# Optimization experiments

Measured on AMD Instinct MI355X. Metric: run time of the kernel, lower is better.

Reference implementation:

```python
import jax, jax.numpy as jnp
import numpy as np

GRID_MIN, GRID_MAX, NUM_GRIDS = -2.0, 2.0, 15
DENOM = (GRID_MAX - GRID_MIN) / (NUM_GRIDS - 1)
LN_EPS = 1e-3  # tf.keras LayerNormalization default epsilon


def setup_inputs() -> dict:
    key = jax.random.key(0)
    k_x, k_sw, k_bw = jax.random.split(key, 3)
    N, D = 32768, 512
    G = NUM_GRIDS
    x = jax.random.normal(k_x, (N, D), dtype=jnp.float32)
    ln_gamma = jnp.ones((D,), dtype=jnp.float32)
    ln_beta = jnp.zeros((D,), dtype=jnp.float32)
    # Glorot-ish scaling to keep outputs sane
    spline_w = jax.random.normal(k_sw, (D, D * G), dtype=jnp.float32) * (1.0 / np.sqrt(D * G))
    base_w = jax.random.normal(k_bw, (D, D), dtype=jnp.float32) * (1.0 / np.sqrt(D))
    base_b = jnp.zeros((D,), dtype=jnp.float32)
    return {"x": x, "ln_gamma": ln_gamma, "ln_beta": ln_beta,
            "spline_w": spline_w, "base_w": base_w, "base_b": base_b}


def reference(x, ln_gamma, ln_beta, spline_w, base_w, base_b):
    N, D = x.shape
    G = NUM_GRIDS
    grid = jnp.linspace(GRID_MIN, GRID_MAX, G).astype(x.dtype)  # non-trainable buffer
    # LayerNorm over last axis (Keras: eps=1e-3)
    mean = jnp.mean(x, axis=-1, keepdims=True)
    var = jnp.mean(jnp.square(x - mean), axis=-1, keepdims=True)
    xn = (x - mean) * jax.lax.rsqrt(var + LN_EPS) * ln_gamma + ln_beta
    # RBF expansion: [N, D, G]
    basis = jnp.exp(-jnp.square((xn[..., None] - grid) / DENOM))
    # Spline GEMM: weight (out, D*G), y = basis_flat @ W^T
    w3 = spline_w.reshape(D, D, G)  # (out, in, grid)
    ret = jnp.einsum('ndg,odg->no', basis, w3)
    # Base residual: Dense(relu(x))
    base = jax.nn.relu(x) @ base_w + base_b
    return ret + base
```

## Files before the change

### kernel.cpp

```cpp
#include <hip/hip_runtime.h>
#include <hip/hip_bf16.h>
#include <stdint.h>

typedef __attribute__((ext_vector_type(8))) short short8;
typedef __attribute__((ext_vector_type(4))) float f32x4;
typedef __attribute__((ext_vector_type(4))) unsigned int u32x4;

#define NROWS 32768
#define DIM 512
#define KTOT 8192
#define KSPL 7680
#define KNEG -17.6730142508898f
#define LNEPS 1e-3f

#if __has_builtin(__builtin_amdgcn_exp2f)
#define EXP2F(x) __builtin_amdgcn_exp2f(x)
#else
#define EXP2F(x) exp2f(x)
#endif

__device__ __forceinline__ unsigned short f2bf(float f) {
    unsigned u = __float_as_uint(f);
    u += 0x7fffu + ((u >> 16) & 1u);
    return (unsigned short)(u >> 16);
}

__device__ __forceinline__ unsigned pack_bf2(float a, float b) {
    unsigned ua = __float_as_uint(a) + 0x8000u;
    unsigned ub = __float_as_uint(b) + 0x8000u;
    return __builtin_amdgcn_perm(ub, ua, 0x07060302u);
}

__global__ __launch_bounds__(256) void prep_w_k(const float* __restrict__ sw,
                                                const float* __restrict__ bwt,
                                                unsigned short* __restrict__ Bw) {
    const int o = blockIdx.x;
    const int t = threadIdx.x;
    const float* swr = sw + (size_t)o * KSPL;
    unsigned short* br = Bw + (size_t)o * KTOT;
    #pragma unroll
    for (int it = 0; it < 30; ++it) {
        int k = it * 256 + t;
        float v = swr[k];
        int d = (unsigned)k / 15u;
        int g = k - d * 15;
        br[(g << 9) + d] = f2bf(v);
    }
    #pragma unroll
    for (int it = 0; it < 2; ++it) {
        int d = it * 256 + t;
        br[KSPL + d] = f2bf(bwt[(size_t)d * DIM + o]);
    }
}

__global__ __launch_bounds__(256) void prep_xn_k(const float* __restrict__ x,
                                                 const float* __restrict__ gam,
                                                 const float* __restrict__ bet,
                                                 unsigned short* __restrict__ xn) {
    const int w = threadIdx.x >> 6, l = threadIdx.x & 63;
    const int row = (blockIdx.x << 2) + w;
    const float* xr = x + (size_t)row * DIM + (l << 3);
    float4 a = *(const float4*)xr;
    float4 b = *(const float4*)(xr + 4);
    float s = a.x + a.y + a.z + a.w + b.x + b.y + b.z + b.w;
    float ss = a.x*a.x + a.y*a.y + a.z*a.z + a.w*a.w
             + b.x*b.x + b.y*b.y + b.z*b.z + b.w*b.w;
    #pragma unroll
    for (int m = 32; m >= 1; m >>= 1) {
        s  += __shfl_xor(s,  m, 64);
        ss += __shfl_xor(ss, m, 64);
    }
    const float mean = s * (1.0f / DIM);
    const float var  = ss * (1.0f / DIM) - mean * mean;
    const float rstd = rsqrtf(var + LNEPS);
    float4 g0 = *(const float4*)(gam + (l << 3));
    float4 g1 = *(const float4*)(gam + (l << 3) + 4);
    float4 b0 = *(const float4*)(bet + (l << 3));
    float4 b1 = *(const float4*)(bet + (l << 3) + 4);
    float e[8];
    e[0] = (a.x - mean) * rstd * g0.x + b0.x;
    e[1] = (a.y - mean) * rstd * g0.y + b0.y;
    e[2] = (a.z - mean) * rstd * g0.z + b0.z;
    e[3] = (a.w - mean) * rstd * g0.w + b0.w;
    e[4] = (b.x - mean) * rstd * g1.x + b1.x;
    e[5] = (b.y - mean) * rstd * g1.y + b1.y;
    e[6] = (b.z - mean) * rstd * g1.z + b1.z;
    e[7] = (b.w - mean) * rstd * g1.w + b1.w;
    u32x4 o;
    o[0] = pack_bf2(e[0], e[1]);
    o[1] = pack_bf2(e[2], e[3]);
    o[2] = pack_bf2(e[4], e[5]);
    o[3] = pack_bf2(e[6], e[7]);
    *(u32x4*)(xn + (size_t)row * DIM + (l << 3)) = o;
}

__global__ __launch_bounds__(512, 4) void kan_gemm(
    const unsigned short* __restrict__ xn,
    const unsigned short* __restrict__ Bw,
    const float* __restrict__ x,
    const float* __restrict__ bb,
    float* __restrict__ out) {
    __shared__ __align__(16) short As[128 * 64];
    __shared__ __align__(16) short Bs[256 * 64];

    const int t = threadIdx.x;
    const int w = t >> 6, l = t & 63;
    const int n0 = (blockIdx.x >> 1) << 7;
    const int o0 = (blockIdx.x & 1) << 8;

    const int kkg = t & 7;
    const int ar  = t >> 3;

    const int wm = (w >> 2) << 6;
    const int wn = (w & 3) << 6;
    const int fm = l & 15, fq = l >> 4;

    const int brow = l >> 3;
    const int bxor = (l & 7) ^ brow;

    f32x4 acc[4][4];
    #pragma unroll
    for (int i = 0; i < 4; ++i)
        #pragma unroll
        for (int j = 0; j < 4; ++j)
            acc[i][j] = (f32x4)0.0f;

    #pragma unroll 1
    for (int dsb = 0; dsb < 8; ++dsb) {
        const int d0 = dsb << 6;
        float xv[2][8];
        #pragma unroll
        for (int i = 0; i < 2; ++i) {
            const int m = ar + (i << 6);
            u32x4 p = *(const u32x4*)(xn + (size_t)(n0 + m) * DIM + d0 + (kkg << 3));
            #pragma unroll
            for (int q = 0; q < 4; ++q) {
                xv[i][2*q]   = __uint_as_float(p[q] << 16);
                xv[i][2*q+1] = __uint_as_float(p[q] & 0xffff0000u);
            }
        }
        #pragma unroll 1
        for (int g = 0; g < 16; ++g) {
            const int kc = (g < 15) ? ((g << 9) + d0) : (KSPL + d0);
            #pragma unroll
            for (int i = 0; i < 4; ++i) {
                const int rb = (i << 6) + (w << 3);
                const unsigned short* gp =
                    Bw + (size_t)(o0 + rb + brow) * KTOT + kc + (bxor << 3);
                __builtin_amdgcn_global_load_lds(
                    (const __attribute__((address_space(1))) void*)gp,
                    (__attribute__((address_space(3))) void*)&Bs[rb << 6],
                    16, 0, 0);
            }
            if (g < 15) {
                const float gv = -2.0f + (float)g * (2.0f / 7.0f);
                #pragma unroll
                for (int i = 0; i < 2; ++i) {
                    const int m = ar + (i << 6);
                    float e[8];
                    #pragma unroll
                    for (int j = 0; j < 8; ++j) {
                        float d = xv[i][j] - gv;
                        e[j] = EXP2F(d * d * KNEG);
                    }
                    u32x4 v;
                    v[0] = pack_bf2(e[0], e[1]);
                    v[1] = pack_bf2(e[2], e[3]);
                    v[2] = pack_bf2(e[4], e[5]);
                    v[3] = pack_bf2(e[6], e[7]);
                    *(u32x4*)&As[((m << 3) | (kkg ^ (m & 7))) << 3] = v;
                }
            } else {
                #pragma unroll
                for (int i = 0; i < 2; ++i) {
                    const int m = ar + (i << 6);
                    const float* xp = x + (size_t)(n0 + m) * DIM + d0 + (kkg << 3);
                    float4 r0 = *(const float4*)xp;
                    float4 r1 = *(const float4*)(xp + 4);
                    u32x4 v;
                    v[0] = pack_bf2(fmaxf(r0.x, 0.f), fmaxf(r0.y, 0.f));
                    v[1] = pack_bf2(fmaxf(r0.z, 0.f), fmaxf(r0.w, 0.f));
                    v[2] = pack_bf2(fmaxf(r1.x, 0.f), fmaxf(r1.y, 0.f));
                    v[3] = pack_bf2(fmaxf(r1.z, 0.f), fmaxf(r1.w, 0.f));
                    *(u32x4*)&As[((m << 3) | (kkg ^ (m & 7))) << 3] = v;
                }
            }
            __syncthreads();
            #pragma unroll
            for (int ks = 0; ks < 2; ++ks) {
                const int kg = (ks << 2) + fq;
                short8 af[4], bf[4];
                #pragma unroll
                for (int mt = 0; mt < 4; ++mt) {
                    const int m = wm + (mt << 4) + fm;
                    af[mt] = *(const short8*)&As[((m << 3) | (kg ^ (m & 7))) << 3];
                }
                #pragma unroll
                for (int nt = 0; nt < 4; ++nt) {
                    const int n = wn + (nt << 4) + fm;
                    bf[nt] = *(const short8*)&Bs[((n << 3) | (kg ^ (n & 7))) << 3];
                }
                #pragma unroll
                for (int mt = 0; mt < 4; ++mt)
                    #pragma unroll
                    for (int nt = 0; nt < 4; ++nt)
                        acc[mt][nt] = __builtin_amdgcn_mfma_f32_16x16x32_bf16(
                            af[mt], bf[nt], acc[mt][nt], 0, 0, 0);
            }
            __syncthreads();
        }
    }
    const int rq = fq << 2;
    float bias[4];
    #pragma unroll
    for (int nt = 0; nt < 4; ++nt) bias[nt] = bb[o0 + wn + (nt << 4) + fm];
    #pragma unroll
    for (int mt = 0; mt < 4; ++mt) {
        #pragma unroll
        for (int nt = 0; nt < 4; ++nt) {
            const int gr = n0 + wm + (mt << 4) + rq;
            const int gc = o0 + wn + (nt << 4) + fm;
            #pragma unroll
            for (int r = 0; r < 4; ++r)
                out[(size_t)(gr + r) * DIM + gc] = acc[mt][nt][r] + bias[nt];
        }
    }
}

extern "C" void kernel_launch(void* const* d_in, const int* in_sizes, int n_in,
                              void* d_out, int out_size, void* d_ws, size_t ws_size,
                              hipStream_t stream) {
    const float* x   = (const float*)d_in[0];
    const float* gam = (const float*)d_in[1];
    const float* bet = (const float*)d_in[2];
    const float* sw  = (const float*)d_in[3];
    const float* bwt = (const float*)d_in[4];
    const float* bb  = (const float*)d_in[5];
    float* out = (float*)d_out;

    unsigned short* Bw = (unsigned short*)d_ws;
    unsigned short* xn = Bw + (size_t)DIM * KTOT;

    prep_w_k<<<dim3(512), dim3(256), 0, stream>>>(sw, bwt, Bw);
    prep_xn_k<<<dim3(NROWS / 4), dim3(256), 0, stream>>>(x, gam, bet, xn);
    kan_gemm<<<dim3(512), dim3(512), 0, stream>>>(xn, Bw, x, bb, out);
}
```

Baseline: 403.9 us.

## Fuse LayerNorm into GEMM, widen tile to full output width

Removes the separate LayerNorm kernel. Each GEMM block now computes the row mean and rstd itself and produces pre-scaled normalized values in fp32, with the exp constant folded into the scale. The block tile grows to 128 rows by all 512 outputs with 1024 threads, so the RBF basis is computed once per row instead of twice, at the cost of a larger B LDS tile and only 256 blocks. The weight prep kernel stages the weights through LDS so the permuted writes become coalesced.

```diff
diff --git a/kernel.cpp b/kernel.cpp
--- a/kernel.cpp
+++ b/kernel.cpp
@@ -10,8 +10,8 @@
 #define DIM 512
 #define KTOT 8192
 #define KSPL 7680
-#define KNEG -17.6730142508898f
 #define LNEPS 1e-3f
+#define SQL 4.20392843f
 
 #if __has_builtin(__builtin_amdgcn_exp2f)
 #define EXP2F(x) __builtin_amdgcn_exp2f(x)
@@ -34,89 +34,66 @@
 __global__ __launch_bounds__(256) void prep_w_k(const float* __restrict__ sw,
                                                 const float* __restrict__ bwt,
                                                 unsigned short* __restrict__ Bw) {
+    __shared__ float lds[KSPL];
     const int o = blockIdx.x;
     const int t = threadIdx.x;
     const float* swr = sw + (size_t)o * KSPL;
     unsigned short* br = Bw + (size_t)o * KTOT;
     #pragma unroll
-    for (int it = 0; it < 30; ++it) {
-        int k = it * 256 + t;
-        float v = swr[k];
-        int d = (unsigned)k / 15u;
-        int g = k - d * 15;
-        br[(g << 9) + d] = f2bf(v);
-    }
+    for (int it = 0; it < 30; ++it) lds[it * 256 + t] = swr[it * 256 + t];
     #pragma unroll
     for (int it = 0; it < 2; ++it) {
         int d = it * 256 + t;
         br[KSPL + d] = f2bf(bwt[(size_t)d * DIM + o]);
     }
-}
-
-__global__ __launch_bounds__(256) void prep_xn_k(const float* __restrict__ x,
-                                                 const float* __restrict__ gam,
-                                                 const float* __restrict__ bet,
-                                                 unsigned short* __restrict__ xn) {
-    const int w = threadIdx.x >> 6, l = threadIdx.x & 63;
-    const int row = (blockIdx.x << 2) + w;
-    const float* xr = x + (size_t)row * DIM + (l << 3);
-    float4 a = *(const float4*)xr;
-    float4 b = *(const float4*)(xr + 4);
-    float s = a.x + a.y + a.z + a.w + b.x + b.y + b.z + b.w;
-    float ss = a.x*a.x + a.y*a.y + a.z*a.z + a.w*a.w
-             + b.x*b.x + b.y*b.y + b.z*b.z + b.w*b.w;
-    #pragma unroll
-    for (int m = 32; m >= 1; m >>= 1) {
-        s  += __shfl_xor(s,  m, 64);
-        ss += __shfl_xor(ss, m, 64);
-    }
-    const float mean = s * (1.0f / DIM);
-    const float var  = ss * (1.0f / DIM) - mean * mean;
-    const float rstd = rsqrtf(var + LNEPS);
-    float4 g0 = *(const float4*)(gam + (l << 3));
-    float4 g1 = *(const float4*)(gam + (l << 3) + 4);
-    float4 b0 = *(const float4*)(bet + (l << 3));
-    float4 b1 = *(const float4*)(bet + (l << 3) + 4);
-    float e[8];
-    e[0] = (a.x - mean) * rstd * g0.x + b0.x;
-    e[1] = (a.y - mean) * rstd * g0.y + b0.y;
-    e[2] = (a.z - mean) * rstd * g0.z + b0.z;
-    e[3] = (a.w - mean) * rstd * g0.w + b0.w;
-    e[4] = (b.x - mean) * rstd * g1.x + b1.x;
-    e[5] = (b.y - mean) * rstd * g1.y + b1.y;
-    e[6] = (b.z - mean) * rstd * g1.z + b1.z;
-    e[7] = (b.w - mean) * rstd * g1.w + b1.w;
-    u32x4 o;
-    o[0] = pack_bf2(e[0], e[1]);
-    o[1] = pack_bf2(e[2], e[3]);
-    o[2] = pack_bf2(e[4], e[5]);
-    o[3] = pack_bf2(e[6], e[7]);
-    *(u32x4*)(xn + (size_t)row * DIM + (l << 3)) = o;
-}
-
-__global__ __launch_bounds__(512, 4) void kan_gemm(
-    const unsigned short* __restrict__ xn,
+    __syncthreads();
+    #pragma unroll
+    for (int it = 0; it < 30; ++it) {
+        int k = it * 256 + t;
+        int g = k >> 9, d = k & 511;
+        br[k] = f2bf(lds[d * 15 + g]);
+    }
+}
+
+__global__ __launch_bounds__(1024, 4) void kan_gemm(
+    const float* __restrict__ x,
     const unsigned short* __restrict__ Bw,
-    const float* __restrict__ x,
+    const float* __restrict__ gam,
+    const float* __restrict__ bet,
     const float* __restrict__ bb,
     float* __restrict__ out) {
     __shared__ __align__(16) short As[128 * 64];
-    __shared__ __align__(16) short Bs[256 * 64];
+    __shared__ __align__(16) short Bs[512 * 64];
 
     const int t = threadIdx.x;
     const int w = t >> 6, l = t & 63;
-    const int n0 = (blockIdx.x >> 1) << 7;
-    const int o0 = (blockIdx.x & 1) << 8;
-
+    const int n0 = blockIdx.x << 7;
+
+    const int ar  = t >> 3;
     const int kkg = t & 7;
-    const int ar  = t >> 3;
-
-    const int wm = (w >> 2) << 6;
-    const int wn = (w & 3) << 6;
+    const int wm = (w >> 3) << 6;
+    const int wn = (w & 7) << 6;
     const int fm = l & 15, fq = l >> 4;
-
     const int brow = l >> 3;
     const int bxor = (l & 7) ^ brow;
+    const int asto = ((ar << 3) | (kkg ^ (ar & 7))) << 3;
+
+    const float* xrow = x + (size_t)(n0 + ar) * DIM;
+    float s = 0.f, ss = 0.f;
+    #pragma unroll
+    for (int it = 0; it < 16; ++it) {
+        float4 v = *(const float4*)(xrow + it * 32 + ((t & 7) << 2));
+        s  += v.x + v.y + v.z + v.w;
+        ss += v.x * v.x + v.y * v.y + v.z * v.z + v.w * v.w;
+    }
+    #pragma unroll
+    for (int m = 4; m >= 1; m >>= 1) {
+        s  += __shfl_xor(s,  m, 64);
+        ss += __shfl_xor(ss, m, 64);
+    }
+    const float mean = s * (1.0f / DIM);
+    const float rstd = rsqrtf(ss * (1.0f / DIM) - mean * mean + LNEPS);
+    const float sr = SQL * rstd;
 
     f32x4 acc[4][4];
     #pragma unroll
@@ -128,15 +105,24 @@
     #pragma unroll 1
     for (int dsb = 0; dsb < 8; ++dsb) {
         const int d0 = dsb << 6;
-        float xv[2][8];
-        #pragma unroll
-        for (int i = 0; i < 2; ++i) {
-            const int m = ar + (i << 6);
-            u32x4 p = *(const u32x4*)(xn + (size_t)(n0 + m) * DIM + d0 + (kkg << 3));
-            #pragma unroll
-            for (int q = 0; q < 4; ++q) {
-                xv[i][2*q]   = __uint_as_float(p[q] << 16);
-                xv[i][2*q+1] = __uint_as_float(p[q] & 0xffff0000u);
+        const int dc = d0 + (kkg << 3);
+        float xr[8], q[8];
+        {
+            float4 a = *(const float4*)(xrow + dc);
+            float4 b = *(const float4*)(xrow + dc + 4);
+            xr[0] = a.x; xr[1] = a.y; xr[2] = a.z; xr[3] = a.w;
+            xr[4] = b.x; xr[5] = b.y; xr[6] = b.z; xr[7] = b.w;
+            float4 g0 = *(const float4*)(gam + dc);
+            float4 g1 = *(const float4*)(gam + dc + 4);
+            float4 b0 = *(const float4*)(bet + dc);
+            float4 b1 = *(const float4*)(bet + dc + 4);
+            float gv[8] = {g0.x, g0.y, g0.z, g0.w, g1.x, g1.y, g1.z, g1.w};
+            float bv[8] = {b0.x, b0.y, b0.z, b0.w, b1.x, b1.y, b1.z, b1.w};
+            #pragma unroll
+            for (int j = 0; j < 8; ++j) {
+                float c = sr * gv[j];
+                float o = __builtin_fmaf(-mean, c, SQL * bv[j]);
+                q[j] = __builtin_fmaf(xr[j], c, o);
             }
         }
         #pragma unroll 1
@@ -144,52 +130,39 @@
             const int kc = (g < 15) ? ((g << 9) + d0) : (KSPL + d0);
             #pragma unroll
             for (int i = 0; i < 4; ++i) {
-                const int rb = (i << 6) + (w << 3);
+                const int rb = (i << 7) + (w << 3);
                 const unsigned short* gp =
-                    Bw + (size_t)(o0 + rb + brow) * KTOT + kc + (bxor << 3);
+                    Bw + (size_t)(rb + brow) * KTOT + kc + (bxor << 3);
                 __builtin_amdgcn_global_load_lds(
                     (const __attribute__((address_space(1))) void*)gp,
                     (__attribute__((address_space(3))) void*)&Bs[rb << 6],
                     16, 0, 0);
             }
+            u32x4 v;
             if (g < 15) {
-                const float gv = -2.0f + (float)g * (2.0f / 7.0f);
-                #pragma unroll
-                for (int i = 0; i < 2; ++i) {
-                    const int m = ar + (i << 6);
-                    float e[8];
-                    #pragma unroll
-                    for (int j = 0; j < 8; ++j) {
-                        float d = xv[i][j] - gv;
-                        e[j] = EXP2F(d * d * KNEG);
-                    }
-                    u32x4 v;
-                    v[0] = pack_bf2(e[0], e[1]);
-                    v[1] = pack_bf2(e[2], e[3]);
-                    v[2] = pack_bf2(e[4], e[5]);
-                    v[3] = pack_bf2(e[6], e[7]);
-                    *(u32x4*)&As[((m << 3) | (kkg ^ (m & 7))) << 3] = v;
+                const float qg = SQL * (-2.0f + (float)g * (2.0f / 7.0f));
+                float e[8];
+                #pragma unroll
+                for (int j = 0; j < 8; ++j) {
+                    float d = q[j] - qg;
+                    e[j] = EXP2F(-(d * d));
                 }
+                v[0] = pack_bf2(e[0], e[1]);
+                v[1] = pack_bf2(e[2], e[3]);
+                v[2] = pack_bf2(e[4], e[5]);
+                v[3] = pack_bf2(e[6], e[7]);
             } else {
-                #pragma unroll
-                for (int i = 0; i < 2; ++i) {
-                    const int m = ar + (i << 6);
-                    const float* xp = x + (size_t)(n0 + m) * DIM + d0 + (kkg << 3);
-                    float4 r0 = *(const float4*)xp;
-                    float4 r1 = *(const float4*)(xp + 4);
-                    u32x4 v;
-                    v[0] = pack_bf2(fmaxf(r0.x, 0.f), fmaxf(r0.y, 0.f));
-                    v[1] = pack_bf2(fmaxf(r0.z, 0.f), fmaxf(r0.w, 0.f));
-                    v[2] = pack_bf2(fmaxf(r1.x, 0.f), fmaxf(r1.y, 0.f));
-                    v[3] = pack_bf2(fmaxf(r1.z, 0.f), fmaxf(r1.w, 0.f));
-                    *(u32x4*)&As[((m << 3) | (kkg ^ (m & 7))) << 3] = v;
-                }
-            }
+                v[0] = pack_bf2(fmaxf(xr[0], 0.f), fmaxf(xr[1], 0.f));
+                v[1] = pack_bf2(fmaxf(xr[2], 0.f), fmaxf(xr[3], 0.f));
+                v[2] = pack_bf2(fmaxf(xr[4], 0.f), fmaxf(xr[5], 0.f));
+                v[3] = pack_bf2(fmaxf(xr[6], 0.f), fmaxf(xr[7], 0.f));
+            }
+            *(u32x4*)&As[asto] = v;
             __syncthreads();
             #pragma unroll
             for (int ks = 0; ks < 2; ++ks) {
                 const int kg = (ks << 2) + fq;
-                short8 af[4], bf[4];
+                short8 af[4], bfr[4];
                 #pragma unroll
                 for (int mt = 0; mt < 4; ++mt) {
                     const int m = wm + (mt << 4) + fm;
@@ -198,14 +171,14 @@
                 #pragma unroll
                 for (int nt = 0; nt < 4; ++nt) {
                     const int n = wn + (nt << 4) + fm;
-                    bf[nt] = *(const short8*)&Bs[((n << 3) | (kg ^ (n & 7))) << 3];
+                    bfr[nt] = *(const short8*)&Bs[((n << 3) | (kg ^ (n & 7))) << 3];
                 }
                 #pragma unroll
                 for (int mt = 0; mt < 4; ++mt)
                     #pragma unroll
                     for (int nt = 0; nt < 4; ++nt)
                         acc[mt][nt] = __builtin_amdgcn_mfma_f32_16x16x32_bf16(
-                            af[mt], bf[nt], acc[mt][nt], 0, 0, 0);
+                            af[mt], bfr[nt], acc[mt][nt], 0, 0, 0);
             }
             __syncthreads();
         }
@@ -213,13 +186,13 @@
     const int rq = fq << 2;
     float bias[4];
     #pragma unroll
-    for (int nt = 0; nt < 4; ++nt) bias[nt] = bb[o0 + wn + (nt << 4) + fm];
+    for (int nt = 0; nt < 4; ++nt) bias[nt] = bb[wn + (nt << 4) + fm];
     #pragma unroll
     for (int mt = 0; mt < 4; ++mt) {
         #pragma unroll
         for (int nt = 0; nt < 4; ++nt) {
             const int gr = n0 + wm + (mt << 4) + rq;
-            const int gc = o0 + wn + (nt << 4) + fm;
+            const int gc = wn + (nt << 4) + fm;
             #pragma unroll
             for (int r = 0; r < 4; ++r)
                 out[(size_t)(gr + r) * DIM + gc] = acc[mt][nt][r] + bias[nt];
@@ -239,9 +212,7 @@
     float* out = (float*)d_out;
 
     unsigned short* Bw = (unsigned short*)d_ws;
-    unsigned short* xn = Bw + (size_t)DIM * KTOT;
 
     prep_w_k<<<dim3(512), dim3(256), 0, stream>>>(sw, bwt, Bw);
-    prep_xn_k<<<dim3(NROWS / 4), dim3(256), 0, stream>>>(x, gam, bet, xn);
-    kan_gemm<<<dim3(512), dim3(512), 0, stream>>>(xn, Bw, x, bb, out);
-}
+    kan_gemm<<<dim3(256), dim3(1024), 0, stream>>>(x, Bw, gam, bet, bb, out);
+}
```

New measurement: 385.6 us. 4.5% less time.
